# Performance work log

Hardware: AMD Instinct MI355X
Metric: run time of the kernel (lower is better)

The kernel has to match this reference:

```python
import jax, jax.numpy as jnp
import numpy as np

B, L = 4, 1024
D_IN, D_MODEL = 2, 512
N_LAYERS, D_STATE, D_CONV, EXPAND, DT_RANK = 2, 16, 4, 2, 32
D_INNER = EXPAND * D_MODEL
EPS = 1e-5


def setup_inputs() -> dict:
    key = jax.random.key(0)
    ks = jax.random.split(key, 10)
    s = 0.02
    return {
        "x": jax.random.normal(ks[0], (B, L, D_IN), jnp.float32),
        "emb_W": jax.random.normal(ks[1], (D_MODEL, D_IN), jnp.float32) * s,
        "emb_b": jnp.zeros((D_MODEL,), jnp.float32),
        "norm_w": jnp.ones((N_LAYERS, D_MODEL), jnp.float32),
        "in_proj_W": jax.random.normal(ks[2], (N_LAYERS, 2 * D_INNER, D_MODEL), jnp.float32) * s,
        "conv_W": jax.random.normal(ks[3], (N_LAYERS, D_INNER, 1, D_CONV), jnp.float32) * s,
        "conv_b": jnp.zeros((N_LAYERS, D_INNER), jnp.float32),
        "x_proj_W": jax.random.normal(ks[4], (N_LAYERS, DT_RANK + 2 * D_STATE, D_INNER), jnp.float32) * s,
        "dt_proj_W": jax.random.normal(ks[5], (N_LAYERS, D_INNER, DT_RANK), jnp.float32) * s,
        "dt_proj_b": jax.random.uniform(ks[6], (N_LAYERS, D_INNER), jnp.float32, -4.0, -2.0),
        "A_log": jnp.log(jnp.broadcast_to(jnp.arange(1, D_STATE + 1, dtype=jnp.float32), (N_LAYERS, D_INNER, D_STATE)) + 0.0),
        "Dskip": jnp.ones((N_LAYERS, D_INNER), jnp.float32),
        "out_proj_W": jax.random.normal(ks[7], (N_LAYERS, D_MODEL, D_INNER), jnp.float32) * s,
        "normf_w": jnp.ones((D_MODEL,), jnp.float32),
    }


def rmsnorm(x, w):
    return x * jax.lax.rsqrt(jnp.mean(x * x, axis=-1, keepdims=True) + EPS) * w


def selective_scan(u, delta, A, Bm, Cm, Dskip):
    # u, delta: (B,L,ED); A: (ED,N); Bm, Cm: (B,L,N); Dskip: (ED,)
    deltaA = jnp.exp(delta[..., None] * A)                      # (B,L,ED,N)
    BX = (delta[..., None] * Bm[:, :, None, :]) * u[..., None]  # (B,L,ED,N)

    def step(h, inp):
        dA, bx, c = inp
        h = dA * h + bx                       # (B,ED,N)
        y = jnp.einsum('ben,bn->be', h, c)    # (B,ED)
        return h, y

    h0 = jnp.zeros((u.shape[0], u.shape[2], A.shape[1]), u.dtype)
    _, ys = jax.lax.scan(step, h0, (deltaA.swapaxes(0, 1), BX.swapaxes(0, 1), Cm.swapaxes(0, 1)))
    y = ys.swapaxes(0, 1)                     # (B,L,ED)
    return y + Dskip * u


def mamba_layer(x, norm_w, ipW, cW, cb, xpW, dtW, dtb, A_log, Dk, opW):
    h = rmsnorm(x, norm_w)
    xz = h @ ipW.T                            # (B,L,2*ED)
    u, z = jnp.split(xz, 2, axis=-1)
    # causal depthwise conv over sequence dim
    uc = jax.lax.conv_general_dilated(
        u.swapaxes(1, 2), cW, window_strides=(1,), padding=[(D_CONV - 1, 0)],
        feature_group_count=D_INNER, dimension_numbers=('NCH', 'OIH', 'NCH'))
    u = jax.nn.silu(uc.swapaxes(1, 2) + cb)   # (B,L,ED)
    xdb = u @ xpW.T                           # (B,L,dt_rank+2N)
    dt, Bm, Cm = jnp.split(xdb, [DT_RANK, DT_RANK + D_STATE], axis=-1)
    delta = jax.nn.softplus(dt @ dtW.T + dtb)
    A = -jnp.exp(A_log)
    y = selective_scan(u, delta, A, Bm, Cm, Dk)
    y = y * jax.nn.silu(z)
    return x + y @ opW.T


def reference(x, emb_W, emb_b, norm_w, in_proj_W, conv_W, conv_b, x_proj_W,
              dt_proj_W, dt_proj_b, A_log, Dskip, out_proj_W, normf_w):
    h = x @ emb_W.T + emb_b                   # (B,L,D_MODEL)
    for l in range(N_LAYERS):
        h = mamba_layer(h, norm_w[l], in_proj_W[l], conv_W[l], conv_b[l],
                        x_proj_W[l], dt_proj_W[l], dt_proj_b[l], A_log[l],
                        Dskip[l], out_proj_W[l])
    return rmsnorm(h, normf_w)
```

## Files before the change

kernel.cpp:

```cpp
#include <hip/hip_runtime.h>
#include <math.h>
#include <stddef.h>

#define BB 4
#define LL 1024
#define DM 512
#define ED 1024
#define NST 16
#define DTR 32
#define XDBC 64
#define BL (BB*LL)
#define CS 16
#define NC 64
#define XKS 16
#define XPAD 68
#define DPAD 132

typedef __attribute__((ext_vector_type(8))) short bf16x8;
typedef __attribute__((ext_vector_type(4))) float f32x4;
typedef unsigned short ushort_t;

__device__ __forceinline__ float silu_f(float x) { return x / (1.f + __expf(-x)); }

__device__ __forceinline__ ushort_t f2b(float f) {
    unsigned int u = __float_as_uint(f);
    unsigned int r = (u + 0x7FFFu + ((u >> 16) & 1u)) >> 16;
    return (ushort_t)r;
}
__device__ __forceinline__ float b2f(ushort_t v) {
    return __uint_as_float(((unsigned int)v) << 16);
}
__device__ __forceinline__ ushort_t f2h(float f) {
    _Float16 h = (_Float16)f;
    return *(ushort_t*)&h;
}
__device__ __forceinline__ float h2f(ushort_t v) {
    _Float16 h = *(_Float16*)&v;
    return (float)h;
}

__device__ __forceinline__ void gload16(const ushort_t* g, ushort_t* l) {
    __builtin_amdgcn_global_load_lds(
        (const __attribute__((address_space(1))) unsigned int*)g,
        (__attribute__((address_space(3))) unsigned int*)l, 16, 0, 0);
}

__global__ void k_init(const float* __restrict__ x, const float* __restrict__ embW,
                       const float* __restrict__ embB, float* __restrict__ h,
                       const float* __restrict__ ipW, const float* __restrict__ opW,
                       ushort_t* __restrict__ wip, ushort_t* __restrict__ wop,
                       int nEmb, int n1, int n2) {
    int i = blockIdx.x * 256 + threadIdx.x;
    if (i < nEmb) {
        int d = i % DM, r = i / DM;
        h[i] = x[r * 2 + 0] * embW[d * 2 + 0] + x[r * 2 + 1] * embW[d * 2 + 1] + embB[d];
        return;
    }
    i -= nEmb;
    const float* src; ushort_t* dst; int q;
    if (i < n1) { src = ipW; dst = wip; q = i; }
    else if (i < n1 + n2) { src = opW; dst = wop; q = i - n1; }
    else return;
    float4 v = *(const float4*)(src + (size_t)q * 4);
    ushort_t o[4] = {f2b(v.x), f2b(v.y), f2b(v.z), f2b(v.w)};
    *(uint2*)(dst + (size_t)q * 4) = *(uint2*)o;
}

template <int BF16OUT>
__global__ __launch_bounds__(256) void k_rmsnorm(const float* __restrict__ in,
                                                 const float* __restrict__ w,
                                                 void* __restrict__ outp) {
    int m = blockIdx.x;
    int tid = threadIdx.x;
    const float* row = in + (size_t)m * DM;
    float2 v = *(const float2*)(row + tid * 2);
    float ss = v.x * v.x + v.y * v.y;
    #pragma unroll
    for (int o = 32; o > 0; o >>= 1) ss += __shfl_down(ss, o, 64);
    __shared__ float red[4];
    int wid = tid >> 6;
    if ((tid & 63) == 0) red[wid] = ss;
    __syncthreads();
    float tot = red[0] + red[1] + red[2] + red[3];
    float rs = rsqrtf(tot * (1.f / DM) + 1e-5f);
    float2 wv = *(const float2*)(w + tid * 2);
    float ox = v.x * rs * wv.x;
    float oy = v.y * rs * wv.y;
    if (BF16OUT) {
        ushort_t o[2] = {f2b(ox), f2b(oy)};
        *(unsigned int*)((ushort_t*)outp + (size_t)m * DM + tid * 2) = *(unsigned int*)o;
    } else {
        *(float2*)((float*)outp + (size_t)m * DM + tid * 2) = make_float2(ox, oy);
    }
}

template <int ADDRES, int BF16OUT, int NT>
__global__ __launch_bounds__(256) void k_bgemm(const ushort_t* __restrict__ A,
                                               const ushort_t* __restrict__ W,
                                               const float* __restrict__ Res,
                                               void* __restrict__ C,
                                               int M, int N, int K, int lda, int ldc) {
    __shared__ ushort_t As[128 * 32];
    __shared__ ushort_t Bs[NT * 32];
    constexpr int NFJ = NT / 32;
    int tid = threadIdx.x;
    int bm = blockIdx.y * 128, bn = blockIdx.x * NT;
    int wave = tid >> 6, lane = tid & 63;
    int wr = wave >> 1, wc = wave & 1;
    int lr = lane & 15;
    int kc = lane >> 4;
    f32x4 acc[4][NFJ];
    #pragma unroll
    for (int i = 0; i < 4; ++i)
        #pragma unroll
        for (int j = 0; j < NFJ; ++j) acc[i][j] = (f32x4){0.f, 0.f, 0.f, 0.f};

    for (int k0 = 0; k0 < K; k0 += 32) {
        __syncthreads();
        #pragma unroll
        for (int ii = 0; ii < 2; ++ii) {
            int g = wave * 128 + ii * 64 + lane;
            int row = g >> 2;
            int c = (g & 3) ^ ((g >> 3) & 3);
            gload16(A + (size_t)(bm + row) * lda + k0 + c * 8,
                    As + (size_t)(wave * 128 + ii * 64) * 8);
        }
        #pragma unroll
        for (int ii = 0; ii < NFJ / 2; ++ii) {
            int g = wave * (NFJ / 2) * 64 + ii * 64 + lane;
            int row = g >> 2;
            int c = (g & 3) ^ ((g >> 3) & 3);
            gload16(W + (size_t)(bn + row) * K + k0 + c * 8,
                    Bs + (size_t)(wave * (NFJ / 2) * 64 + ii * 64) * 8);
        }
        __syncthreads();
        bf16x8 af[4], bfr[NFJ];
        #pragma unroll
        for (int i = 0; i < 4; ++i) {
            int ra = wr * 64 + i * 16 + lr;
            int ca = kc ^ ((ra >> 1) & 3);
            af[i] = *(const bf16x8*)(As + ra * 32 + ca * 8);
        }
        #pragma unroll
        for (int j = 0; j < NFJ; ++j) {
            int rb = wc * (NT / 2) + j * 16 + lr;
            int cb = kc ^ ((rb >> 1) & 3);
            bfr[j] = *(const bf16x8*)(Bs + rb * 32 + cb * 8);
        }
        #pragma unroll
        for (int i = 0; i < 4; ++i)
            #pragma unroll
            for (int j = 0; j < NFJ; ++j)
                acc[i][j] = __builtin_amdgcn_mfma_f32_16x16x32_bf16(af[i], bfr[j], acc[i][j], 0, 0, 0);
    }
    int crow0 = bm + wr * 64 + (lane >> 4) * 4;
    #pragma unroll
    for (int i = 0; i < 4; ++i)
        #pragma unroll
        for (int j = 0; j < NFJ; ++j)
            #pragma unroll
            for (int r = 0; r < 4; ++r) {
                size_t off = (size_t)(crow0 + i * 16 + r) * ldc + bn + wc * (NT / 2) + j * 16 + lr;
                float v = acc[i][j][r];
                if (ADDRES) v += Res[off];
                if (BF16OUT) ((ushort_t*)C)[off] = f2b(v);
                else         ((float*)C)[off] = v;
            }
}

__global__ __launch_bounds__(256) void k_cxp(const ushort_t* __restrict__ xzb,
                                             const float* __restrict__ cw,
                                             const float* __restrict__ cb,
                                             const float* __restrict__ xpW,
                                             ushort_t* __restrict__ ub,
                                             float* __restrict__ Pp) {
    __shared__ float As[64][XPAD];
    __shared__ float Ws[64][XPAD];
    int tid = threadIdx.x;
    int ks = blockIdx.x;
    int bm = blockIdx.y * 64;
    int ec0 = ks * 64;

    {
        int r0 = (tid >> 4) * 4;
        int e4 = (tid & 15) * 4;
        int e = ec0 + e4;
        float cw4[4][4], cb4[4];
        #pragma unroll
        for (int j = 0; j < 4; ++j) {
            float4 w = *(const float4*)(cw + (size_t)(e + j) * 4);
            cw4[j][0] = w.x; cw4[j][1] = w.y; cw4[j][2] = w.z; cw4[j][3] = w.w;
        }
        float4 cbv = *(const float4*)(cb + e);
        cb4[0] = cbv.x; cb4[1] = cbv.y; cb4[2] = cbv.z; cb4[3] = cbv.w;
        #pragma unroll
        for (int i = 0; i < 4; ++i) {
            int row = bm + r0 + i;
            int tloc = row & (LL - 1);
            const ushort_t* xrow = xzb + (size_t)row * 2048 + e;
            uint2 z2 = make_uint2(0, 0);
            uint2 v3 = *(const uint2*)xrow;
            uint2 v2 = (tloc >= 1) ? *(const uint2*)(xrow - 2048) : z2;
            uint2 v1 = (tloc >= 2) ? *(const uint2*)(xrow - 4096) : z2;
            uint2 v0 = (tloc >= 3) ? *(const uint2*)(xrow - 6144) : z2;
            const ushort_t* p0 = (const ushort_t*)&v0;
            const ushort_t* p1 = (const ushort_t*)&v1;
            const ushort_t* p2 = (const ushort_t*)&v2;
            const ushort_t* p3 = (const ushort_t*)&v3;
            ushort_t ures[4];
            #pragma unroll
            for (int j = 0; j < 4; ++j) {
                float a = cb4[j] + b2f(p0[j]) * cw4[j][0] + b2f(p1[j]) * cw4[j][1]
                                 + b2f(p2[j]) * cw4[j][2] + b2f(p3[j]) * cw4[j][3];
                float uu = silu_f(a);
                As[e4 + j][r0 + i] = uu;
                ures[j] = f2b(uu);
            }
            *(uint2*)(ub + (size_t)row * ED + e) = *(uint2*)ures;
        }
    }
    {
        int r = tid >> 2;
        int kc = (tid & 3) * 16;
        const float4* wp = (const float4*)(xpW + (size_t)r * ED + ec0 + kc);
        #pragma unroll
        for (int i = 0; i < 4; ++i) {
            float4 wv = wp[i];
            Ws[kc + i * 4 + 0][r] = wv.x; Ws[kc + i * 4 + 1][r] = wv.y;
            Ws[kc + i * 4 + 2][r] = wv.z; Ws[kc + i * 4 + 3][r] = wv.w;
        }
    }
    __syncthreads();
    int tm = (tid >> 4) * 4;
    int tn = (tid & 15) * 4;
    float acc[4][4] = {};
    #pragma unroll 4
    for (int k = 0; k < 64; ++k) {
        float4 a = *(const float4*)&As[k][tm];
        float4 b = *(const float4*)&Ws[k][tn];
        acc[0][0] += a.x * b.x; acc[0][1] += a.x * b.y; acc[0][2] += a.x * b.z; acc[0][3] += a.x * b.w;
        acc[1][0] += a.y * b.x; acc[1][1] += a.y * b.y; acc[1][2] += a.y * b.z; acc[1][3] += a.y * b.w;
        acc[2][0] += a.z * b.x; acc[2][1] += a.z * b.y; acc[2][2] += a.z * b.z; acc[2][3] += a.z * b.w;
        acc[3][0] += a.w * b.x; acc[3][1] += a.w * b.y; acc[3][2] += a.w * b.z; acc[3][3] += a.w * b.w;
    }
    float* pp = Pp + (size_t)ks * BL * XDBC;
    #pragma unroll
    for (int i = 0; i < 4; ++i)
        *(float4*)(pp + (size_t)(bm + tm + i) * XDBC + tn) =
            make_float4(acc[i][0], acc[i][1], acc[i][2], acc[i][3]);
}

__global__ void k_xred(const float* __restrict__ Pp, float* __restrict__ xdb) {
    int i = blockIdx.x * 256 + threadIdx.x;
    float4 s = make_float4(0.f, 0.f, 0.f, 0.f);
    #pragma unroll
    for (int sl = 0; sl < XKS; ++sl) {
        float4 v = *(const float4*)(Pp + (size_t)sl * BL * XDBC + (size_t)i * 4);
        s.x += v.x; s.y += v.y; s.z += v.z; s.w += v.w;
    }
    *(float4*)(xdb + (size_t)i * 4) = s;
}

__global__ __launch_bounds__(256) void k_delta(const float* __restrict__ xdb,
                                               const float* __restrict__ dtW,
                                               const float* __restrict__ dtb,
                                               ushort_t* __restrict__ dyh) {
    __shared__ float Dt[32][DPAD];
    __shared__ float Wt[32][DPAD];
    int tid = threadIdx.x;
    int bm = blockIdx.y * 128;
    int bn = blockIdx.x * 128;
    int r = tid >> 1;
    int hh = (tid & 1) * 16;
    const float4* dp = (const float4*)(xdb + (size_t)(bm + r) * XDBC + hh);
    const float4* wp = (const float4*)(dtW + (size_t)(bn + r) * 32 + hh);
    #pragma unroll
    for (int i = 0; i < 4; ++i) {
        float4 v = dp[i];
        Dt[hh + i * 4 + 0][r] = v.x; Dt[hh + i * 4 + 1][r] = v.y;
        Dt[hh + i * 4 + 2][r] = v.z; Dt[hh + i * 4 + 3][r] = v.w;
        float4 w = wp[i];
        Wt[hh + i * 4 + 0][r] = w.x; Wt[hh + i * 4 + 1][r] = w.y;
        Wt[hh + i * 4 + 2][r] = w.z; Wt[hh + i * 4 + 3][r] = w.w;
    }
    __syncthreads();
    int tm = (tid >> 4) * 8;
    int tn = (tid & 15) * 8;
    float acc[8][8] = {};
    #pragma unroll 8
    for (int k = 0; k < 32; ++k) {
        float4 a0 = *(const float4*)&Dt[k][tm];
        float4 a1 = *(const float4*)&Dt[k][tm + 4];
        float4 b0 = *(const float4*)&Wt[k][tn];
        float4 b1 = *(const float4*)&Wt[k][tn + 4];
        float a[8] = {a0.x, a0.y, a0.z, a0.w, a1.x, a1.y, a1.z, a1.w};
        float b[8] = {b0.x, b0.y, b0.z, b0.w, b1.x, b1.y, b1.z, b1.w};
        #pragma unroll
        for (int i = 0; i < 8; ++i)
            #pragma unroll
            for (int j = 0; j < 8; ++j) acc[i][j] += a[i] * b[j];
    }
    float4 t0 = *(const float4*)(dtb + bn + tn);
    float4 t1 = *(const float4*)(dtb + bn + tn + 4);
    float bias[8] = {t0.x, t0.y, t0.z, t0.w, t1.x, t1.y, t1.z, t1.w};
    #pragma unroll
    for (int i = 0; i < 8; ++i) {
        ushort_t o16[8];
        #pragma unroll
        for (int j = 0; j < 8; ++j) {
            float v = acc[i][j] + bias[j];
            v = (v > 20.f) ? v : __logf(1.f + __expf(v));
            o16[j] = f2h(v);
        }
        size_t off = (size_t)(bm + tm + i) * ED + bn + tn;
        *(uint4*)(dyh + off) = *(uint4*)o16;
    }
}

__global__ __launch_bounds__(256) void k_scan1(const ushort_t* __restrict__ dyh,
                                               const ushort_t* __restrict__ u,
                                               const float* __restrict__ xdb,
                                               const float* __restrict__ A_log,
                                               float* __restrict__ P,
                                               float* __restrict__ S) {
    int tid = threadIdx.x;
    int e = ((blockIdx.x & 3) << 8) + tid;
    int c = (blockIdx.x >> 2) & (NC - 1);
    int b = blockIdx.x >> 8;
    float Ac[16];
    const float4* ap = (const float4*)(A_log + (size_t)e * NST);
    #pragma unroll
    for (int q = 0; q < 4; ++q) {
        float4 a = ap[q];
        Ac[q * 4 + 0] = -__expf(a.x); Ac[q * 4 + 1] = -__expf(a.y);
        Ac[q * 4 + 2] = -__expf(a.z); Ac[q * 4 + 3] = -__expf(a.w);
    }
    float h[16] = {};
    float s = 0.f;
    const ushort_t* dp = dyh + ((size_t)b * LL + c * CS) * ED + e;
    const ushort_t* up = u + ((size_t)b * LL + c * CS) * ED + e;
    const float* xp = xdb + ((size_t)b * LL + c * CS) * XDBC;
    for (int tt = 0; tt < CS; ++tt) {
        float dv = h2f(dp[(size_t)tt * ED]);
        float uv = b2f(up[(size_t)tt * ED]);
        s += dv;
        float du = dv * uv;
        const float4* bp = (const float4*)(xp + tt * XDBC + DTR);
        #pragma unroll
        for (int q = 0; q < 4; ++q) {
            float4 bv = bp[q];
            h[q * 4 + 0] = __expf(dv * Ac[q * 4 + 0]) * h[q * 4 + 0] + du * bv.x;
            h[q * 4 + 1] = __expf(dv * Ac[q * 4 + 1]) * h[q * 4 + 1] + du * bv.y;
            h[q * 4 + 2] = __expf(dv * Ac[q * 4 + 2]) * h[q * 4 + 2] + du * bv.z;
            h[q * 4 + 3] = __expf(dv * Ac[q * 4 + 3]) * h[q * 4 + 3] + du * bv.w;
        }
    }
    float4* pp = (float4*)(P + ((size_t)(b * NC + c) * ED + e) * NST);
    pp[0] = make_float4(h[0], h[1], h[2], h[3]);
    pp[1] = make_float4(h[4], h[5], h[6], h[7]);
    pp[2] = make_float4(h[8], h[9], h[10], h[11]);
    pp[3] = make_float4(h[12], h[13], h[14], h[15]);
    S[(size_t)(b * NC + c) * ED + e] = s;
}

__global__ __launch_bounds__(256) void k_scan2(float* __restrict__ P,
                                               const float* __restrict__ S,
                                               const float* __restrict__ A_log) {
    int i = blockIdx.x * 256 + threadIdx.x;
    int n = i & 15;
    int e = (i >> 4) & (ED - 1);
    int b = i >> 14;
    float Ac = -__expf(A_log[(size_t)e * NST + n]);
    float hin = 0.f;
    for (int c = 0; c < NC; ++c) {
        size_t base = (size_t)(b * NC + c) * ED + e;
        float p = P[base * NST + n];
        float s = S[base];
        P[base * NST + n] = hin;
        hin = __expf(Ac * s) * hin + p;
    }
}

__global__ __launch_bounds__(256) void k_scan3(const ushort_t* __restrict__ dyh,
                                               const ushort_t* __restrict__ u,
                                               const float* __restrict__ xdb,
                                               const ushort_t* __restrict__ xzb,
                                               const float* __restrict__ A_log,
                                               const float* __restrict__ Dskip,
                                               const float* __restrict__ P,
                                               ushort_t* __restrict__ yb) {
    int tid = threadIdx.x;
    int e = ((blockIdx.x & 3) << 8) + tid;
    int c = (blockIdx.x >> 2) & (NC - 1);
    int b = blockIdx.x >> 8;
    float Ac[16], h[16];
    const float4* ap = (const float4*)(A_log + (size_t)e * NST);
    #pragma unroll
    for (int q = 0; q < 4; ++q) {
        float4 a = ap[q];
        Ac[q * 4 + 0] = -__expf(a.x); Ac[q * 4 + 1] = -__expf(a.y);
        Ac[q * 4 + 2] = -__expf(a.z); Ac[q * 4 + 3] = -__expf(a.w);
    }
    const float4* pp = (const float4*)(P + ((size_t)(b * NC + c) * ED + e) * NST);
    #pragma unroll
    for (int q = 0; q < 4; ++q) {
        float4 hv = pp[q];
        h[q * 4 + 0] = hv.x; h[q * 4 + 1] = hv.y;
        h[q * 4 + 2] = hv.z; h[q * 4 + 3] = hv.w;
    }
    float Dk = Dskip[e];
    const ushort_t* dp = dyh + ((size_t)b * LL + c * CS) * ED + e;
    const ushort_t* up = u + ((size_t)b * LL + c * CS) * ED + e;
    const float* xp = xdb + ((size_t)b * LL + c * CS) * XDBC;
    const ushort_t* zp = xzb + ((size_t)b * LL + c * CS) * 2048 + 1024 + e;
    ushort_t* yp = yb + ((size_t)b * LL + c * CS) * ED + e;
    for (int tt = 0; tt < CS; ++tt) {
        float dv = h2f(dp[(size_t)tt * ED]);
        float uv = b2f(up[(size_t)tt * ED]);
        float zv = b2f(zp[(size_t)tt * 2048]);
        float du = dv * uv;
        const float4* bp = (const float4*)(xp + tt * XDBC + DTR);
        const float4* cp = (const float4*)(xp + tt * XDBC + DTR + NST);
        float y = 0.f;
        #pragma unroll
        for (int q = 0; q < 4; ++q) {
            float4 bv = bp[q];
            float4 cv = cp[q];
            h[q * 4 + 0] = __expf(dv * Ac[q * 4 + 0]) * h[q * 4 + 0] + du * bv.x;
            h[q * 4 + 1] = __expf(dv * Ac[q * 4 + 1]) * h[q * 4 + 1] + du * bv.y;
            h[q * 4 + 2] = __expf(dv * Ac[q * 4 + 2]) * h[q * 4 + 2] + du * bv.z;
            h[q * 4 + 3] = __expf(dv * Ac[q * 4 + 3]) * h[q * 4 + 3] + du * bv.w;
            y += h[q * 4 + 0] * cv.x + h[q * 4 + 1] * cv.y +
                 h[q * 4 + 2] * cv.z + h[q * 4 + 3] * cv.w;
        }
        yp[(size_t)tt * ED] = f2b((y + Dk * uv) * silu_f(zv));
    }
}

extern "C" void kernel_launch(void* const* d_in, const int* in_sizes, int n_in,
                              void* d_out, int out_size, void* d_ws, size_t ws_size,
                              hipStream_t stream) {
    const float* x     = (const float*)d_in[0];
    const float* embW  = (const float*)d_in[1];
    const float* embB  = (const float*)d_in[2];
    const float* normw = (const float*)d_in[3];
    const float* ipW   = (const float*)d_in[4];
    const float* cW    = (const float*)d_in[5];
    const float* cb    = (const float*)d_in[6];
    const float* xpW   = (const float*)d_in[7];
    const float* dtW   = (const float*)d_in[8];
    const float* dtb   = (const float*)d_in[9];
    const float* Alog  = (const float*)d_in[10];
    const float* Dsk   = (const float*)d_in[11];
    const float* opW   = (const float*)d_in[12];
    const float* normfw= (const float*)d_in[13];
    float* out = (float*)d_out;

    float* ws  = (float*)d_ws;
    float* h   = ws;
    ushort_t* xzb = (ushort_t*)(h + (size_t)BL * DM);
    ushort_t* ub  = xzb + (size_t)BL * 2 * ED;
    float* xdb = (float*)(ub + (size_t)BL * ED);
    float* Pp  = xdb + (size_t)BL * XDBC;
    float* S   = Pp + (size_t)XKS * BL * XDBC;
    ushort_t* wip = (ushort_t*)(S + (size_t)BB * NC * ED);
    ushort_t* wop = wip + (size_t)2 * 2 * ED * DM;
    ushort_t* yb  = wop + (size_t)2 * DM * ED;
    float* P      = Pp;
    ushort_t* hnb = (ushort_t*)d_out;
    ushort_t* dyh = (ushort_t*)d_out;

    int nEmb = BL * DM;
    int n1 = 2 * 2 * ED * DM / 4, n2 = 2 * DM * ED / 4;
    k_init<<<(nEmb + n1 + n2 + 255) / 256, 256, 0, stream>>>(
        x, embW, embB, h, ipW, opW, wip, wop, nEmb, n1, n2);

    for (int l = 0; l < 2; ++l) {
        const float* Al = Alog + (size_t)l * ED * NST;
        k_rmsnorm<1><<<BL, 256, 0, stream>>>(h, normw + (size_t)l * DM, hnb);
        k_bgemm<0, 1, 128><<<dim3(2 * ED / 128, BL / 128), 256, 0, stream>>>(
            hnb, wip + (size_t)l * 2 * ED * DM, nullptr, xzb, BL, 2 * ED, DM, DM, 2 * ED);
        k_cxp<<<dim3(XKS, BL / 64), 256, 0, stream>>>(
            xzb, cW + (size_t)l * ED * 4, cb + (size_t)l * ED,
            xpW + (size_t)l * XDBC * ED, ub, Pp);
        k_xred<<<BL * XDBC / 4 / 256, 256, 0, stream>>>(Pp, xdb);
        k_delta<<<dim3(ED / 128, BL / 128), 256, 0, stream>>>(
            xdb, dtW + (size_t)l * ED * DTR, dtb + (size_t)l * ED, dyh);
        k_scan1<<<BB * NC * (ED / 256), 256, 0, stream>>>(dyh, ub, xdb, Al, P, S);
        k_scan2<<<BB * ED * NST / 256, 256, 0, stream>>>(P, S, Al);
        k_scan3<<<BB * NC * (ED / 256), 256, 0, stream>>>(
            dyh, ub, xdb, xzb, Al, Dsk + (size_t)l * ED, P, yb);
        k_bgemm<1, 0, 64><<<dim3(DM / 64, BL / 128), 256, 0, stream>>>(
            yb, wop + (size_t)l * DM * ED, h, h, BL, DM, ED, ED, DM);
    }
    k_rmsnorm<0><<<BL, 256, 0, stream>>>(h, normfw, out);
}
```

Measured before the change: 273.9 us.

## Fuse dt projection and softplus into scan kernels, store chunk states in bf16

Removes the separate k_delta GEMM and recomputes delta (dt_proj plus softplus) inside both scan passes. Each thread holds its row of dt weights in registers and reads xdb rows from a shared-memory tile. This avoids writing and reading back the fp16 delta tensor. The chunk carry states P are also stored as bf16 instead of fp32 to halve their traffic. The cost is redundant dt-projection work in scan1 and scan3, higher register pressure, and lower precision for the carried states.

```diff
diff --git a/kernel.cpp b/kernel.cpp
--- a/kernel.cpp
+++ b/kernel.cpp
@@ -14,7 +14,6 @@
 #define NC 64
 #define XKS 16
 #define XPAD 68
-#define DPAD 132
 
 typedef __attribute__((ext_vector_type(8))) short bf16x8;
 typedef __attribute__((ext_vector_type(4))) float f32x4;
@@ -29,14 +28,6 @@
 }
 __device__ __forceinline__ float b2f(ushort_t v) {
     return __uint_as_float(((unsigned int)v) << 16);
-}
-__device__ __forceinline__ ushort_t f2h(float f) {
-    _Float16 h = (_Float16)f;
-    return *(ushort_t*)&h;
-}
-__device__ __forceinline__ float h2f(ushort_t v) {
-    _Float16 h = *(_Float16*)&v;
-    return (float)h;
 }
 
 __device__ __forceinline__ void gload16(const ushort_t* g, ushort_t* l) {
@@ -261,72 +252,23 @@
     *(float4*)(xdb + (size_t)i * 4) = s;
 }
 
-__global__ __launch_bounds__(256) void k_delta(const float* __restrict__ xdb,
+__global__ __launch_bounds__(256) void k_scan1(const float* __restrict__ xdb,
+                                               const ushort_t* __restrict__ u,
                                                const float* __restrict__ dtW,
                                                const float* __restrict__ dtb,
-                                               ushort_t* __restrict__ dyh) {
-    __shared__ float Dt[32][DPAD];
-    __shared__ float Wt[32][DPAD];
-    int tid = threadIdx.x;
-    int bm = blockIdx.y * 128;
-    int bn = blockIdx.x * 128;
-    int r = tid >> 1;
-    int hh = (tid & 1) * 16;
-    const float4* dp = (const float4*)(xdb + (size_t)(bm + r) * XDBC + hh);
-    const float4* wp = (const float4*)(dtW + (size_t)(bn + r) * 32 + hh);
-    #pragma unroll
-    for (int i = 0; i < 4; ++i) {
-        float4 v = dp[i];
-        Dt[hh + i * 4 + 0][r] = v.x; Dt[hh + i * 4 + 1][r] = v.y;
-        Dt[hh + i * 4 + 2][r] = v.z; Dt[hh + i * 4 + 3][r] = v.w;
-        float4 w = wp[i];
-        Wt[hh + i * 4 + 0][r] = w.x; Wt[hh + i * 4 + 1][r] = w.y;
-        Wt[hh + i * 4 + 2][r] = w.z; Wt[hh + i * 4 + 3][r] = w.w;
-    }
-    __syncthreads();
-    int tm = (tid >> 4) * 8;
-    int tn = (tid & 15) * 8;
-    float acc[8][8] = {};
-    #pragma unroll 8
-    for (int k = 0; k < 32; ++k) {
-        float4 a0 = *(const float4*)&Dt[k][tm];
-        float4 a1 = *(const float4*)&Dt[k][tm + 4];
-        float4 b0 = *(const float4*)&Wt[k][tn];
-        float4 b1 = *(const float4*)&Wt[k][tn + 4];
-        float a[8] = {a0.x, a0.y, a0.z, a0.w, a1.x, a1.y, a1.z, a1.w};
-        float b[8] = {b0.x, b0.y, b0.z, b0.w, b1.x, b1.y, b1.z, b1.w};
-        #pragma unroll
-        for (int i = 0; i < 8; ++i)
-            #pragma unroll
-            for (int j = 0; j < 8; ++j) acc[i][j] += a[i] * b[j];
-    }
-    float4 t0 = *(const float4*)(dtb + bn + tn);
-    float4 t1 = *(const float4*)(dtb + bn + tn + 4);
-    float bias[8] = {t0.x, t0.y, t0.z, t0.w, t1.x, t1.y, t1.z, t1.w};
-    #pragma unroll
-    for (int i = 0; i < 8; ++i) {
-        ushort_t o16[8];
-        #pragma unroll
-        for (int j = 0; j < 8; ++j) {
-            float v = acc[i][j] + bias[j];
-            v = (v > 20.f) ? v : __logf(1.f + __expf(v));
-            o16[j] = f2h(v);
-        }
-        size_t off = (size_t)(bm + tm + i) * ED + bn + tn;
-        *(uint4*)(dyh + off) = *(uint4*)o16;
-    }
-}
-
-__global__ __launch_bounds__(256) void k_scan1(const ushort_t* __restrict__ dyh,
-                                               const ushort_t* __restrict__ u,
-                                               const float* __restrict__ xdb,
                                                const float* __restrict__ A_log,
-                                               float* __restrict__ P,
+                                               ushort_t* __restrict__ P,
                                                float* __restrict__ S) {
+    __shared__ float Xs[CS][XDBC];
     int tid = threadIdx.x;
     int e = ((blockIdx.x & 3) << 8) + tid;
     int c = (blockIdx.x >> 2) & (NC - 1);
     int b = blockIdx.x >> 8;
+    size_t r0 = (size_t)b * LL + c * CS;
+    {
+        int t = tid >> 4, q = (tid & 15) * 4;
+        *(float4*)&Xs[t][q] = *(const float4*)(xdb + (r0 + t) * XDBC + q);
+    }
     float Ac[16];
     const float4* ap = (const float4*)(A_log + (size_t)e * NST);
     #pragma unroll
@@ -335,35 +277,56 @@
         Ac[q * 4 + 0] = -__expf(a.x); Ac[q * 4 + 1] = -__expf(a.y);
         Ac[q * 4 + 2] = -__expf(a.z); Ac[q * 4 + 3] = -__expf(a.w);
     }
+    float dtw[32];
+    const float4* wq = (const float4*)(dtW + (size_t)e * DTR);
+    #pragma unroll
+    for (int q = 0; q < 8; ++q) {
+        float4 w = wq[q];
+        dtw[q * 4 + 0] = w.x; dtw[q * 4 + 1] = w.y;
+        dtw[q * 4 + 2] = w.z; dtw[q * 4 + 3] = w.w;
+    }
+    float bias = dtb[e];
+    __syncthreads();
+    float dv[CS];
+    #pragma unroll
+    for (int t = 0; t < CS; ++t) {
+        float acc = bias;
+        #pragma unroll
+        for (int q = 0; q < 8; ++q) {
+            float4 d = *(const float4*)&Xs[t][q * 4];
+            acc += d.x * dtw[q * 4 + 0] + d.y * dtw[q * 4 + 1] +
+                   d.z * dtw[q * 4 + 2] + d.w * dtw[q * 4 + 3];
+        }
+        dv[t] = (acc > 20.f) ? acc : __logf(1.f + __expf(acc));
+    }
     float h[16] = {};
     float s = 0.f;
-    const ushort_t* dp = dyh + ((size_t)b * LL + c * CS) * ED + e;
-    const ushort_t* up = u + ((size_t)b * LL + c * CS) * ED + e;
-    const float* xp = xdb + ((size_t)b * LL + c * CS) * XDBC;
+    const ushort_t* up = u + r0 * ED + e;
     for (int tt = 0; tt < CS; ++tt) {
-        float dv = h2f(dp[(size_t)tt * ED]);
+        float d = dv[tt];
         float uv = b2f(up[(size_t)tt * ED]);
-        s += dv;
-        float du = dv * uv;
-        const float4* bp = (const float4*)(xp + tt * XDBC + DTR);
+        s += d;
+        float du = d * uv;
+        const float4* bp = (const float4*)&Xs[tt][DTR];
         #pragma unroll
         for (int q = 0; q < 4; ++q) {
             float4 bv = bp[q];
-            h[q * 4 + 0] = __expf(dv * Ac[q * 4 + 0]) * h[q * 4 + 0] + du * bv.x;
-            h[q * 4 + 1] = __expf(dv * Ac[q * 4 + 1]) * h[q * 4 + 1] + du * bv.y;
-            h[q * 4 + 2] = __expf(dv * Ac[q * 4 + 2]) * h[q * 4 + 2] + du * bv.z;
-            h[q * 4 + 3] = __expf(dv * Ac[q * 4 + 3]) * h[q * 4 + 3] + du * bv.w;
-        }
-    }
-    float4* pp = (float4*)(P + ((size_t)(b * NC + c) * ED + e) * NST);
-    pp[0] = make_float4(h[0], h[1], h[2], h[3]);
-    pp[1] = make_float4(h[4], h[5], h[6], h[7]);
-    pp[2] = make_float4(h[8], h[9], h[10], h[11]);
-    pp[3] = make_float4(h[12], h[13], h[14], h[15]);
+            h[q * 4 + 0] = __expf(d * Ac[q * 4 + 0]) * h[q * 4 + 0] + du * bv.x;
+            h[q * 4 + 1] = __expf(d * Ac[q * 4 + 1]) * h[q * 4 + 1] + du * bv.y;
+            h[q * 4 + 2] = __expf(d * Ac[q * 4 + 2]) * h[q * 4 + 2] + du * bv.z;
+            h[q * 4 + 3] = __expf(d * Ac[q * 4 + 3]) * h[q * 4 + 3] + du * bv.w;
+        }
+    }
+    ushort_t pb[16];
+    #pragma unroll
+    for (int n = 0; n < 16; ++n) pb[n] = f2b(h[n]);
+    uint4* pp = (uint4*)(P + ((size_t)(b * NC + c) * ED + e) * NST);
+    pp[0] = ((uint4*)pb)[0];
+    pp[1] = ((uint4*)pb)[1];
     S[(size_t)(b * NC + c) * ED + e] = s;
 }
 
-__global__ __launch_bounds__(256) void k_scan2(float* __restrict__ P,
+__global__ __launch_bounds__(256) void k_scan2(ushort_t* __restrict__ P,
                                                const float* __restrict__ S,
                                                const float* __restrict__ A_log) {
     int i = blockIdx.x * 256 + threadIdx.x;
@@ -374,26 +337,33 @@
     float hin = 0.f;
     for (int c = 0; c < NC; ++c) {
         size_t base = (size_t)(b * NC + c) * ED + e;
-        float p = P[base * NST + n];
+        float p = b2f(P[base * NST + n]);
         float s = S[base];
-        P[base * NST + n] = hin;
+        P[base * NST + n] = f2b(hin);
         hin = __expf(Ac * s) * hin + p;
     }
 }
 
-__global__ __launch_bounds__(256) void k_scan3(const ushort_t* __restrict__ dyh,
+__global__ __launch_bounds__(256) void k_scan3(const float* __restrict__ xdb,
                                                const ushort_t* __restrict__ u,
-                                               const float* __restrict__ xdb,
                                                const ushort_t* __restrict__ xzb,
+                                               const float* __restrict__ dtW,
+                                               const float* __restrict__ dtb,
                                                const float* __restrict__ A_log,
                                                const float* __restrict__ Dskip,
-                                               const float* __restrict__ P,
+                                               const ushort_t* __restrict__ P,
                                                ushort_t* __restrict__ yb) {
+    __shared__ float Xs[CS][XDBC];
     int tid = threadIdx.x;
     int e = ((blockIdx.x & 3) << 8) + tid;
     int c = (blockIdx.x >> 2) & (NC - 1);
     int b = blockIdx.x >> 8;
-    float Ac[16], h[16];
+    size_t r0 = (size_t)b * LL + c * CS;
+    {
+        int t = tid >> 4, q = (tid & 15) * 4;
+        *(float4*)&Xs[t][q] = *(const float4*)(xdb + (r0 + t) * XDBC + q);
+    }
+    float Ac[16];
     const float4* ap = (const float4*)(A_log + (size_t)e * NST);
     #pragma unroll
     for (int q = 0; q < 4; ++q) {
@@ -401,35 +371,55 @@
         Ac[q * 4 + 0] = -__expf(a.x); Ac[q * 4 + 1] = -__expf(a.y);
         Ac[q * 4 + 2] = -__expf(a.z); Ac[q * 4 + 3] = -__expf(a.w);
     }
-    const float4* pp = (const float4*)(P + ((size_t)(b * NC + c) * ED + e) * NST);
-    #pragma unroll
-    for (int q = 0; q < 4; ++q) {
-        float4 hv = pp[q];
-        h[q * 4 + 0] = hv.x; h[q * 4 + 1] = hv.y;
-        h[q * 4 + 2] = hv.z; h[q * 4 + 3] = hv.w;
-    }
+    float dtw[32];
+    const float4* wq = (const float4*)(dtW + (size_t)e * DTR);
+    #pragma unroll
+    for (int q = 0; q < 8; ++q) {
+        float4 w = wq[q];
+        dtw[q * 4 + 0] = w.x; dtw[q * 4 + 1] = w.y;
+        dtw[q * 4 + 2] = w.z; dtw[q * 4 + 3] = w.w;
+    }
+    float bias = dtb[e];
+    __syncthreads();
+    float dv[CS];
+    #pragma unroll
+    for (int t = 0; t < CS; ++t) {
+        float acc = bias;
+        #pragma unroll
+        for (int q = 0; q < 8; ++q) {
+            float4 d = *(const float4*)&Xs[t][q * 4];
+            acc += d.x * dtw[q * 4 + 0] + d.y * dtw[q * 4 + 1] +
+                   d.z * dtw[q * 4 + 2] + d.w * dtw[q * 4 + 3];
+        }
+        dv[t] = (acc > 20.f) ? acc : __logf(1.f + __expf(acc));
+    }
+    float h[16];
+    const uint4* pp4 = (const uint4*)(P + ((size_t)(b * NC + c) * ED + e) * NST);
+    uint4 pA = pp4[0], pB = pp4[1];
+    const ushort_t* pw0 = (const ushort_t*)&pA;
+    const ushort_t* pw1 = (const ushort_t*)&pB;
+    #pragma unroll
+    for (int n = 0; n < 8; ++n) { h[n] = b2f(pw0[n]); h[8 + n] = b2f(pw1[n]); }
     float Dk = Dskip[e];
-    const ushort_t* dp = dyh + ((size_t)b * LL + c * CS) * ED + e;
-    const ushort_t* up = u + ((size_t)b * LL + c * CS) * ED + e;
-    const float* xp = xdb + ((size_t)b * LL + c * CS) * XDBC;
-    const ushort_t* zp = xzb + ((size_t)b * LL + c * CS) * 2048 + 1024 + e;
-    ushort_t* yp = yb + ((size_t)b * LL + c * CS) * ED + e;
+    const ushort_t* up = u + r0 * ED + e;
+    const ushort_t* zp = xzb + r0 * 2048 + 1024 + e;
+    ushort_t* yp = yb + r0 * ED + e;
     for (int tt = 0; tt < CS; ++tt) {
-        float dv = h2f(dp[(size_t)tt * ED]);
+        float d = dv[tt];
         float uv = b2f(up[(size_t)tt * ED]);
         float zv = b2f(zp[(size_t)tt * 2048]);
-        float du = dv * uv;
-        const float4* bp = (const float4*)(xp + tt * XDBC + DTR);
-        const float4* cp = (const float4*)(xp + tt * XDBC + DTR + NST);
+        float du = d * uv;
+        const float4* bp = (const float4*)&Xs[tt][DTR];
+        const float4* cp = (const float4*)&Xs[tt][DTR + NST];
         float y = 0.f;
         #pragma unroll
         for (int q = 0; q < 4; ++q) {
             float4 bv = bp[q];
             float4 cv = cp[q];
-            h[q * 4 + 0] = __expf(dv * Ac[q * 4 + 0]) * h[q * 4 + 0] + du * bv.x;
-            h[q * 4 + 1] = __expf(dv * Ac[q * 4 + 1]) * h[q * 4 + 1] + du * bv.y;
-            h[q * 4 + 2] = __expf(dv * Ac[q * 4 + 2]) * h[q * 4 + 2] + du * bv.z;
-            h[q * 4 + 3] = __expf(dv * Ac[q * 4 + 3]) * h[q * 4 + 3] + du * bv.w;
+            h[q * 4 + 0] = __expf(d * Ac[q * 4 + 0]) * h[q * 4 + 0] + du * bv.x;
+            h[q * 4 + 1] = __expf(d * Ac[q * 4 + 1]) * h[q * 4 + 1] + du * bv.y;
+            h[q * 4 + 2] = __expf(d * Ac[q * 4 + 2]) * h[q * 4 + 2] + du * bv.z;
+            h[q * 4 + 3] = __expf(d * Ac[q * 4 + 3]) * h[q * 4 + 3] + du * bv.w;
             y += h[q * 4 + 0] * cv.x + h[q * 4 + 1] * cv.y +
                  h[q * 4 + 2] * cv.z + h[q * 4 + 3] * cv.w;
         }
@@ -466,9 +456,8 @@
     ushort_t* wip = (ushort_t*)(S + (size_t)BB * NC * ED);
     ushort_t* wop = wip + (size_t)2 * 2 * ED * DM;
     ushort_t* yb  = wop + (size_t)2 * DM * ED;
-    float* P      = Pp;
+    ushort_t* P   = (ushort_t*)Pp;
     ushort_t* hnb = (ushort_t*)d_out;
-    ushort_t* dyh = (ushort_t*)d_out;
 
     int nEmb = BL * DM;
     int n1 = 2 * 2 * ED * DM / 4, n2 = 2 * DM * ED / 4;
@@ -477,6 +466,8 @@
 
     for (int l = 0; l < 2; ++l) {
         const float* Al = Alog + (size_t)l * ED * NST;
+        const float* dtWl = dtW + (size_t)l * ED * DTR;
+        const float* dtbl = dtb + (size_t)l * ED;
         k_rmsnorm<1><<<BL, 256, 0, stream>>>(h, normw + (size_t)l * DM, hnb);
         k_bgemm<0, 1, 128><<<dim3(2 * ED / 128, BL / 128), 256, 0, stream>>>(
             hnb, wip + (size_t)l * 2 * ED * DM, nullptr, xzb, BL, 2 * ED, DM, DM, 2 * ED);
@@ -484,12 +475,11 @@
             xzb, cW + (size_t)l * ED * 4, cb + (size_t)l * ED,
             xpW + (size_t)l * XDBC * ED, ub, Pp);
         k_xred<<<BL * XDBC / 4 / 256, 256, 0, stream>>>(Pp, xdb);
-        k_delta<<<dim3(ED / 128, BL / 128), 256, 0, stream>>>(
-            xdb, dtW + (size_t)l * ED * DTR, dtb + (size_t)l * ED, dyh);
-        k_scan1<<<BB * NC * (ED / 256), 256, 0, stream>>>(dyh, ub, xdb, Al, P, S);
+        k_scan1<<<BB * NC * (ED / 256), 256, 0, stream>>>(
+            xdb, ub, dtWl, dtbl, Al, P, S);
         k_scan2<<<BB * ED * NST / 256, 256, 0, stream>>>(P, S, Al);
         k_scan3<<<BB * NC * (ED / 256), 256, 0, stream>>>(
-            dyh, ub, xdb, xzb, Al, Dsk + (size_t)l * ED, P, yb);
+            xdb, ub, xzb, dtWl, dtbl, Al, Dsk + (size_t)l * ED, P, yb);
         k_bgemm<1, 0, 64><<<dim3(DM / 64, BL / 128), 256, 0, stream>>>(
             yb, wop + (size_t)l * DM * ED, h, h, BL, DM, ED, ED, DM);
     }
```

Result: no change. 274.4 us (+0.2%).
